# Performance work log

Measured on AMD Instinct MI355X. Metric: run time of the kernel, lower is better.

Reference implementation:

```python
import jax, jax.numpy as jnp
import numpy as np

B, N, INC, H, W = 1, 6, 256, 56, 100
DD, CC = 41, 64                         # depth bins (4..45 step 1), cam feat channels
NX, NY, NZ = 33, 33, 2                  # BEV grid from pc_range=[-50,-50,-5,50,50,3], grid=3
CZ = CC * NZ                            # 128 channels into bevencode
DXV = jnp.array([3.0, 3.0, 3.0], jnp.float32)
BXV = jnp.array([-48.5, -48.5, -3.5], jnp.float32)


def _frustum():
    ds = jnp.arange(4.0, 45.0, 1.0)                      # (41,)
    xs = jnp.linspace(0.0, 1599.0, W)
    ys = jnp.linspace(0.0, 899.0, H)
    d = jnp.broadcast_to(ds[:, None, None], (DD, H, W))
    xg = jnp.broadcast_to(xs[None, None, :], (DD, H, W))
    yg = jnp.broadcast_to(ys[None, :, None], (DD, H, W))
    return jnp.stack([xg, yg, d], -1)                    # (D,H,W,3)


def _conv(x, w):
    return jax.lax.conv_general_dilated(x, w, (1, 1), 'SAME',
                                        dimension_numbers=('NCHW', 'OIHW', 'NCHW'))


def _bn_relu(x, s, b, m, v):
    inv = s / jnp.sqrt(v + 1e-5)
    return jax.nn.relu(x * inv[None, :, None, None] + (b - m * inv)[None, :, None, None])


def _forward(x, rots, trans, dn_w, dn_b,
             bw1, bn1_s, bn1_b, bn1_m, bn1_v,
             bw2, bn2_s, bn2_b, bn2_m, bn2_v,
             bw3, bn3_s, bn3_b, bn3_m, bn3_v,
             bw4, bn4_s, bn4_b, bn4_m, bn4_v):
    # ---- CamEncode: 1x1 depthnet -> softmax depth dist + context features ----
    xf = x.reshape(B * N, INC, H, W)
    y = _conv(xf, dn_w) + dn_b[None, :, None, None]
    depth = jax.nn.softmax(y[:, :DD], axis=1).reshape(B, N, DD, H, W)
    feat = y[:, DD:DD + CC].reshape(B, N, CC, H, W)
    # ---- get_geometry: (u*d, v*d, d) -> ego frame ----
    fr = _frustum()                                                     # (D,H,W,3)
    pts = jnp.concatenate([fr[..., :2] * fr[..., 2:3], fr[..., 2:3]], -1)
    geom = jnp.einsum('bnij,dhwj->bndhwi', rots, pts) + trans[:, :, None, None, None, :]
    # ---- voxel indices (torch .long() truncates toward zero) ----
    coor = ((geom - (BXV - DXV / 2.0)) / DXV).astype(jnp.int32)         # (B,N,D,H,W,3)
    cx, cy, cz = coor[..., 0], coor[..., 1], coor[..., 2]
    kept = (cx >= 0) & (cx < NX) & (cy >= 0) & (cy < NY) & (cz >= 0) & (cz < NZ)
    bidx = jnp.arange(B, dtype=jnp.int32)[:, None, None, None, None]
    ranks = ((bidx * NZ + cz) * NY + cy) * NX + cx                      # bev rank per point
    nvox = B * NZ * NY * NX
    seg = jnp.where(kept, ranks, nvox).reshape(-1)                      # drop bucket = nvox
    # ---- lift: depth-weighted outer product, splat: segment-sum by voxel ----
    vol = depth[..., None] * feat.transpose(0, 1, 3, 4, 2)[:, :, None]  # (B,N,D,H,W,C)
    bev = jax.ops.segment_sum(vol.reshape(-1, CC), seg, num_segments=nvox + 1)[:nvox]
    bev = bev.reshape(B, NZ, NY, NX, CC).transpose(0, 4, 1, 2, 3).reshape(B, CZ, NY, NX)
    h = _bn_relu(_conv(bev, bw1), bn1_s, bn1_b, bn1_m, bn1_v)
    h = _bn_relu(_conv(h, bw2), bn2_s, bn2_b, bn2_m, bn2_v)
    h = _bn_relu(_conv(h, bw3), bn3_s, bn3_b, bn3_m, bn3_v)
    h = _bn_relu(_conv(h, bw4), bn4_s, bn4_b, bn4_m, bn4_v)
    return h                                                            # (B,256,33,33)


def setup_inputs() -> dict:
    key = jax.random.key(0)
    ks = jax.random.split(key, 16)
    x = jax.random.normal(ks[0], (B, N, INC, H, W), jnp.float32)
    # rots = small rotation perturbation composed with intrinsics inverse
    kinv = jnp.array([[1.0 / 800.0, 0.0, -1.0], [0.0, 1.0 / 800.0, -0.5625], [0.0, 0.0, 1.0]], jnp.float32)
    R = jnp.eye(3, dtype=jnp.float32) + 0.05 * jax.random.normal(ks[1], (B, N, 3, 3), jnp.float32)
    rots = jnp.einsum('bnij,jk->bnik', R, kinv)
    trans = 2.0 * jax.random.normal(ks[2], (B, N, 3), jnp.float32)

    def w(k, o, i, kh, kw):
        return jax.random.normal(k, (o, i, kh, kw), jnp.float32) * (2.0 / (i * kh * kw)) ** 0.5

    def bn(k, c):
        k1, k2, k3, k4 = jax.random.split(k, 4)
        return (1.0 + 0.1 * jax.random.normal(k1, (c,), jnp.float32),
                0.1 * jax.random.normal(k2, (c,), jnp.float32),
                0.1 * jax.random.normal(k3, (c,), jnp.float32),
                jax.random.uniform(k4, (c,), jnp.float32, 0.5, 1.5))
    bn1 = bn(ks[7], CZ); bn2 = bn(ks[8], 512); bn3 = bn(ks[9], 512); bn4 = bn(ks[10], 256)
    return dict(
        x=x, rots=rots, trans=trans,
        dn_w=w(ks[3], DD + CC, INC, 1, 1), dn_b=jnp.zeros((DD + CC,), jnp.float32),
        bw1=w(ks[4], CZ, CZ, 3, 3),
        bn1_s=bn1[0], bn1_b=bn1[1], bn1_m=bn1[2], bn1_v=bn1[3],
        bw2=w(ks[5], 512, CZ, 3, 3),
        bn2_s=bn2[0], bn2_b=bn2[1], bn2_m=bn2[2], bn2_v=bn2[3],
        bw3=w(ks[6], 512, 512, 3, 3),
        bn3_s=bn3[0], bn3_b=bn3[1], bn3_m=bn3[2], bn3_v=bn3[3],
        bw4=w(ks[11], 256, 512, 3, 3),
        bn4_s=bn4[0], bn4_b=bn4[1], bn4_m=bn4[2], bn4_v=bn4[3])


def reference(x, rots, trans, dn_w, dn_b,
              bw1, bn1_s, bn1_b, bn1_m, bn1_v,
              bw2, bn2_s, bn2_b, bn2_m, bn2_v,
              bw3, bn3_s, bn3_b, bn3_m, bn3_v,
              bw4, bn4_s, bn4_b, bn4_m, bn4_v):
    return _forward(x, rots, trans, dn_w, dn_b,
                    bw1, bn1_s, bn1_b, bn1_m, bn1_v,
                    bw2, bn2_s, bn2_b, bn2_m, bn2_v,
                    bw3, bn3_s, bn3_b, bn3_m, bn3_v,
                    bw4, bn4_s, bn4_b, bn4_m, bn4_v)
```

## Files before the change

### kernel.cpp

```cpp
#include <hip/hip_runtime.h>
#include <math.h>

#define NCAM  6
#define INC   256
#define HH    56
#define WW    100
#define HW    5600
#define NPIX  33600
#define DDEP  41
#define CFEAT 64
#define NCH   105
#define NXG   33
#define NYG   33
#define NZG   2
#define NVOX  2178
#define PADW  35
#define PADHW 1225
#define NPIXO 1089

typedef short bf16x8 __attribute__((ext_vector_type(8)));
typedef float f32x4  __attribute__((ext_vector_type(4)));

#define Y_OFF    0
#define Y_SZ     (NCAM * NCH * HW)
#define WDH_OFF  (Y_OFF + Y_SZ)
#define WDL_OFF  (WDH_OFF + 16384)
#define W1H_OFF  (WDL_OFF + 16384)
#define W1L_OFF  (W1H_OFF + 73728)
#define W2H_OFF  (W1L_OFF + 73728)
#define W2L_OFF  (W2H_OFF + 294912)
#define W3H_OFF  (W2L_OFF + 294912)
#define W3L_OFF  (W3H_OFF + 1179648)
#define W4H_OFF  (W3L_OFF + 1179648)
#define W4L_OFF  (W4H_OFF + 589824)
#define BEV_OFF  (W4L_OFF + 589824)
#define BEV_SZ   (NVOX * CFEAT)
#define A0H_OFF  (BEV_OFF + BEV_SZ)
#define A0L_OFF  (A0H_OFF + 78400)
#define A1H_OFF  (A0L_OFF + 78400)
#define A1L_OFF  (A1H_OFF + 78400)
#define A2H_OFF  (A1L_OFF + 78400)
#define A2L_OFF  (A2H_OFF + 313600)
#define A3H_OFF  (A2L_OFF + 313600)
#define A3L_OFF  (A3H_OFF + 313600)
#define P_OFF    (A3L_OFF + 313600)
#define P_SZ     4460544
#define WS_END   (P_OFF + P_SZ)

__device__ __forceinline__ unsigned short f2bf_rn(float f) {
    unsigned u = __builtin_bit_cast(unsigned, f);
    unsigned r = (u + 0x7FFFu + ((u >> 16) & 1u)) >> 16;
    return (unsigned short)r;
}
__device__ __forceinline__ void split_bf(float f, unsigned short& h, unsigned short& l) {
    h = f2bf_rn(f);
    float hf = __builtin_bit_cast(float, (unsigned)h << 16);
    l = f2bf_rn(f - hf);
}
__device__ __forceinline__ void split_bf_trunc(float f, short& h, short& l) {
    unsigned u = __builtin_bit_cast(unsigned, f);
    h = (short)(u >> 16);
    float hf = __builtin_bit_cast(float, u & 0xFFFF0000u);
    float r = f - hf;
    l = (short)(__builtin_bit_cast(unsigned, r) >> 16);
}

__device__ __forceinline__ void wprep_conv(const float* __restrict__ wgt,
                                           unsigned short* __restrict__ wh,
                                           unsigned short* __restrict__ wl,
                                           int COUT, int CIN, int i)
{
    int jj = i & 7, lane = (i >> 3) & 63;
    int r  = i >> 9;
    int nchk = CIN >> 5;
    int chk = r % nchk; r /= nchk;
    int ncog = COUT >> 4;
    int cog = r % ncog; int dydx = r / ncog;
    int co = cog * 16 + (lane & 15);
    int ci = chk * 32 + (lane >> 4) * 8 + jj;
    float w = wgt[((size_t)co * CIN + ci) * 9 + dydx];
    unsigned short h, l; split_bf(w, h, l);
    wh[i] = h; wl[i] = l;
}

__global__ __launch_bounds__(256) void k_wprep_all(const float* __restrict__ dnw,
                                                   const float* __restrict__ bw1,
                                                   const float* __restrict__ bw2,
                                                   const float* __restrict__ bw3,
                                                   const float* __restrict__ bw4,
                                                   unsigned short* __restrict__ wdh,
                                                   unsigned short* __restrict__ wdl,
                                                   unsigned short* __restrict__ w1h,
                                                   unsigned short* __restrict__ w1l,
                                                   unsigned short* __restrict__ w2h,
                                                   unsigned short* __restrict__ w2l,
                                                   unsigned short* __restrict__ w3h,
                                                   unsigned short* __restrict__ w3l,
                                                   unsigned short* __restrict__ w4h,
                                                   unsigned short* __restrict__ w4l)
{
    int i = blockIdx.x * 256 + threadIdx.x;
    if (i < 32768) {
        int jj = i & 7, lane = (i >> 3) & 63, chk = (i >> 9) & 7, ct = i >> 12;
        int co = ct * 16 + (lane & 15);
        int ci = chk * 32 + (lane >> 4) * 8 + jj;
        float w = (co < NCH) ? dnw[co * 256 + ci] : 0.f;
        unsigned short h, l; split_bf(w, h, l);
        wdh[i] = h; wdl[i] = l;
        return;
    }
    i -= 32768;
    if (i < 147456)  { wprep_conv(bw1, w1h, w1l, 128, 128, i); return; }
    i -= 147456;
    if (i < 589824)  { wprep_conv(bw2, w2h, w2l, 512, 128, i); return; }
    i -= 589824;
    if (i < 2359296) { wprep_conv(bw3, w3h, w3l, 512, 512, i); return; }
    i -= 2359296;
    if (i < 1179648) { wprep_conv(bw4, w4h, w4l, 256, 512, i); return; }
}

__global__ __launch_bounds__(256) void k_depthnet_fused(const float* __restrict__ x,
                                                        const unsigned short* __restrict__ wdh,
                                                        const unsigned short* __restrict__ wdl,
                                                        const float* __restrict__ dnb,
                                                        float* __restrict__ y)
{
    const int t  = threadIdx.x;
    const int w  = t >> 6;
    const int l  = t & 63;
    const int lp = l & 15;
    const int q  = l >> 4;
    const int n   = blockIdx.y;
    const int px  = blockIdx.x * 64 + w * 16 + lp;
    const bool pok = px < HW;
    const float* xl = x + (size_t)n * INC * HW + (pok ? px : 0);

    f32x4 acc[7];
#pragma unroll
    for (int ct = 0; ct < 7; ++ct) acc[ct] = (f32x4){0.f, 0.f, 0.f, 0.f};

#pragma unroll 2
    for (int ci0 = 0; ci0 < INC; ci0 += 32) {
        float bv[8];
#pragma unroll
        for (int jj = 0; jj < 8; ++jj)
            bv[jj] = xl[(size_t)(ci0 + q * 8 + jj) * HW];
        bf16x8 Bh, Bl;
#pragma unroll
        for (int jj = 0; jj < 8; ++jj) {
            short h, lo; split_bf_trunc(pok ? bv[jj] : 0.f, h, lo);
            Bh[jj] = h; Bl[jj] = lo;
        }
#pragma unroll
        for (int ct = 0; ct < 7; ++ct) {
            const size_t ab = (size_t)((ct * 8 + (ci0 >> 5)) * 64 + l) * 8;
            bf16x8 Ah = *(const bf16x8*)&wdh[ab];
            bf16x8 Al = *(const bf16x8*)&wdl[ab];
            acc[ct] = __builtin_amdgcn_mfma_f32_16x16x32_bf16(Ah, Bh, acc[ct], 0, 0, 0);
            acc[ct] = __builtin_amdgcn_mfma_f32_16x16x32_bf16(Ah, Bl, acc[ct], 0, 0, 0);
            acc[ct] = __builtin_amdgcn_mfma_f32_16x16x32_bf16(Al, Bh, acc[ct], 0, 0, 0);
        }
    }

    float v[4][4];
#pragma unroll
    for (int ct = 0; ct < 4; ++ct)
#pragma unroll
        for (int j = 0; j < 4; ++j) {
            int co = ct * 16 + q * 4 + j;
            v[ct][j] = acc[ct][j] + dnb[co];
        }

    {
        float m = -3.4e38f;
#pragma unroll
        for (int ct = 0; ct < 4; ++ct)
#pragma unroll
            for (int j = 0; j < 4; ++j) {
                int co = ct * 16 + q * 4 + j;
                if (co < DDEP) m = fmaxf(m, v[ct][j]);
            }
        m = fmaxf(m, __shfl_xor(m, 16));
        m = fmaxf(m, __shfl_xor(m, 32));
        float s = 0.f;
        float e[4][4];
#pragma unroll
        for (int ct = 0; ct < 4; ++ct)
#pragma unroll
            for (int j = 0; j < 4; ++j) {
                int co = ct * 16 + q * 4 + j;
                e[ct][j] = (co < DDEP) ? expf(v[ct][j] - m) : 0.f;
                s += e[ct][j];
            }
        s += __shfl_xor(s, 16);
        s += __shfl_xor(s, 32);
#pragma unroll
        for (int ct = 0; ct < 4; ++ct)
#pragma unroll
            for (int j = 0; j < 4; ++j) {
                int co = ct * 16 + q * 4 + j;
                if (co < DDEP) v[ct][j] = e[ct][j] / s;
            }
    }

    if (pok) {
#pragma unroll
        for (int ct = 0; ct < 4; ++ct)
#pragma unroll
            for (int j = 0; j < 4; ++j) {
                int co = ct * 16 + q * 4 + j;
                y[((size_t)n * NCH + co) * HW + px] = v[ct][j];
            }
#pragma unroll
        for (int ct = 4; ct < 7; ++ct)
#pragma unroll
            for (int j = 0; j < 4; ++j) {
                int co = ct * 16 + q * 4 + j;
                if (co < NCH)
                    y[((size_t)n * NCH + co) * HW + px] = acc[ct][j] + dnb[co];
            }
    }
}

__global__ __launch_bounds__(256) void k_splat2(const float* __restrict__ y,
                                                const float* __restrict__ rots,
                                                const float* __restrict__ trans,
                                                float* __restrict__ bev)
{
    __shared__ int vox[32 * DDEP];
    const int t  = threadIdx.x;
    const int p0 = blockIdx.x * 32;

    for (int k = t; k < 32 * DDEP; k += 256) {
        int pl = k / DDEP, d = k - pl * DDEP;
        int p = p0 + pl;
        int vx = -1;
        {
            int n = p / HW, hw = p - n * HW;
            int wi = hw % WW, hi = hw / WW;
            const float su = 1599.0f / 99.0f;
            const float sv = 899.0f / 55.0f;
            float u = __fmul_rn((float)wi, su);
            float v = __fmul_rn((float)hi, sv);
            const float* r = rots + n * 9;
            const float* tr = trans + n * 3;
            float dd  = 4.0f + (float)d;
            float pxv = __fmul_rn(u, dd);
            float pyv = __fmul_rn(v, dd);
            float gx = __fadd_rn(__fadd_rn(__fadd_rn(__fmul_rn(r[0], pxv), __fmul_rn(r[1], pyv)), __fmul_rn(r[2], dd)), tr[0]);
            float gy = __fadd_rn(__fadd_rn(__fadd_rn(__fmul_rn(r[3], pxv), __fmul_rn(r[4], pyv)), __fmul_rn(r[5], dd)), tr[1]);
            float gz = __fadd_rn(__fadd_rn(__fadd_rn(__fmul_rn(r[6], pxv), __fmul_rn(r[7], pyv)), __fmul_rn(r[8], dd)), tr[2]);
            int cx = (int)__fdiv_rn(__fadd_rn(gx, 50.0f), 3.0f);
            int cy = (int)__fdiv_rn(__fadd_rn(gy, 50.0f), 3.0f);
            int cz = (int)__fdiv_rn(__fadd_rn(gz, 5.0f), 3.0f);
            if (cx >= 0 && cx < NXG && cy >= 0 && cy < NYG && cz >= 0 && cz < NZG)
                vx = (cz * NYG + cy) * NXG + cx;
        }
        vox[k] = vx;
    }
    __syncthreads();

    const int g  = t >> 5;
    const int pl = t & 31;
    const int p  = p0 + pl;
    int n = p / HW, hw = p - n * HW;
    const float* dbase = y + (size_t)n * NCH * HW + hw;
    const float* fbase = dbase + (size_t)DDEP * HW;
    float f[8];
#pragma unroll
    for (int j = 0; j < 8; ++j) f[j] = fbase[(size_t)(g * 8 + j) * HW];

    float a[8];
#pragma unroll
    for (int j = 0; j < 8; ++j) a[j] = 0.f;
    int cur = -1;
    for (int d = 0; d < DDEP; ++d) {
        int vx = vox[pl * DDEP + d];
        if (vx != cur) {
            if (cur >= 0) {
                float* vp = bev + (size_t)cur * CFEAT + g * 8;
#pragma unroll
                for (int j = 0; j < 8; ++j) atomicAdd(vp + j, a[j]);
            }
            cur = vx;
#pragma unroll
            for (int j = 0; j < 8; ++j) a[j] = 0.f;
        }
        if (vx >= 0) {
            float dval = dbase[(size_t)d * HW];
#pragma unroll
            for (int j = 0; j < 8; ++j) a[j] += __fmul_rn(dval, f[j]);
        }
    }
    if (cur >= 0) {
        float* vp = bev + (size_t)cur * CFEAT + g * 8;
#pragma unroll
        for (int j = 0; j < 8; ++j) atomicAdd(vp + j, a[j]);
    }
}

__global__ __launch_bounds__(256) void k_bev2act(const float* __restrict__ bev,
                                                 unsigned short* __restrict__ ah,
                                                 unsigned short* __restrict__ al)
{
    int i = blockIdx.x * 256 + threadIdx.x;
    if (i >= NVOX * CFEAT) return;
    int vx = i >> 6, c = i & 63;
    int cz = vx / NPIXO, rem = vx - cz * NPIXO;
    int yy = rem / NXG, xx = rem - yy * NXG;
    int ch = c * 2 + cz;
    int pos = (yy + 1) * PADW + xx + 1;
    unsigned short h, l; split_bf(bev[i], h, l);
    ah[pos * 128 + ch] = h;
    al[pos * 128 + ch] = l;
}

template<int CIN, int COUT, int SL>
__global__ __launch_bounds__(256) void k_conv_mfma(const unsigned short* __restrict__ ah,
                                                   const unsigned short* __restrict__ al,
                                                   const unsigned short* __restrict__ wh,
                                                   const unsigned short* __restrict__ wl,
                                                   float* __restrict__ P)
{
    constexpr int CI_PER = CIN / SL;
    constexpr int CHUNKS = CI_PER / 32;
    constexpr int NSLOT  = CHUNKS * 8;
    constexpr int SMASK  = NSLOT - 1;
    constexpr int ROW    = CHUNKS * 64;
    constexpr int NCOB = COUT / 64;
    constexpr int G    = NCOB * SL;
    constexpr int GX   = G / 8;
    constexpr int POSN = 140;
    __shared__ unsigned short bs[POSN * ROW];
    const int t  = threadIdx.x;
    const int w  = t >> 6;
    const int l  = t & 63;
    const int lp = l & 15;
    const int q  = l >> 4;

    const int bid   = blockIdx.x;
    const int xcd   = bid & 7;
    const int slot  = bid >> 3;
    const int ytile = slot % 17;
    const int gon   = slot / 17;
    const int group = xcd * GX + gon;
    const int cobi  = group % NCOB;
    const int sl    = group / NCOB;

    const int y0  = ytile * 2;
    const int cob = cobi * 64 + w * 16;
    const int ci_base = sl * CI_PER;

    int  pos0[5];
    bool vld[5];
#pragma unroll
    for (int ct = 0; ct < 5; ++ct) {
        int tp = ct * 16 + lp;
        int r = tp / 33, c = tp - r * 33;
        bool v = (tp < 66) && (y0 + r < 33);
        vld[ct]  = v;
        pos0[ct] = v ? (r * 35 + c) : 0;
    }

    for (int i = t; i < POSN * NSLOT; i += 256) {
        int pos = i / NSLOT, s = i - pos * NSLOT;
        int gpos = y0 * 35 + pos;
        bool hi = s < CHUNKS * 4;
        int sq = hi ? s : s - CHUNKS * 4;
        int cio = (sq >> 2) * 32 + (sq & 3) * 8;
        const unsigned short* src = hi ? ah : al;
        int sp = s ^ (pos & SMASK);
        uint4 val = make_uint4(0u, 0u, 0u, 0u);
        if (gpos < PADHW)
            val = *(const uint4*)&src[(size_t)gpos * CIN + ci_base + cio];
        *(uint4*)&bs[pos * ROW + sp * 8] = val;
    }
    __syncthreads();

    f32x4 acc[5];
#pragma unroll
    for (int ct = 0; ct < 5; ++ct) acc[ct] = (f32x4){0.f, 0.f, 0.f, 0.f};

#pragma unroll 3
    for (int dydx = 0; dydx < 9; ++dydx) {
        int dy = dydx / 3, dx = dydx - dy * 3;
        int off = dy * 35 + dx;
        bf16x8 Ah[CHUNKS], Al[CHUNKS];
#pragma unroll
        for (int c = 0; c < CHUNKS; ++c) {
            const size_t abase = (size_t)(((dydx * (COUT >> 4) + (cob >> 4)) * (CIN >> 5)
                                           + (ci_base >> 5) + c) * 64 + l) * 8;
            Ah[c] = *(const bf16x8*)&wh[abase];
            Al[c] = *(const bf16x8*)&wl[abase];
        }
#pragma unroll
        for (int ct = 0; ct < 5; ++ct) {
            int pos = pos0[ct] + off;
#pragma unroll
            for (int c = 0; c < CHUNKS; ++c) {
                int sph = (c * 4 + q) ^ (pos & SMASK);
                bf16x8 Bh = *(const bf16x8*)&bs[pos * ROW + sph * 8];
                bf16x8 Bl = *(const bf16x8*)&bs[pos * ROW + (sph ^ (CHUNKS * 4)) * 8];
                acc[ct] = __builtin_amdgcn_mfma_f32_16x16x32_bf16(Ah[c], Bh, acc[ct], 0, 0, 0);
                acc[ct] = __builtin_amdgcn_mfma_f32_16x16x32_bf16(Ah[c], Bl, acc[ct], 0, 0, 0);
                acc[ct] = __builtin_amdgcn_mfma_f32_16x16x32_bf16(Al[c], Bh, acc[ct], 0, 0, 0);
            }
        }
    }

#pragma unroll
    for (int ct = 0; ct < 5; ++ct) {
        if (!vld[ct]) continue;
        int gp = y0 * 33 + ct * 16 + lp;
        float* dst = P + ((size_t)sl * NPIXO + gp) * COUT + cob + q * 4;
        *(f32x4*)dst = acc[ct];
    }
}

template<int SL>
__global__ __launch_bounds__(256) void k_finish(const float* __restrict__ P,
                                                const float* __restrict__ bns,
                                                const float* __restrict__ bnb,
                                                const float* __restrict__ bnm,
                                                const float* __restrict__ bnv,
                                                unsigned short* __restrict__ oh,
                                                unsigned short* __restrict__ ol,
                                                float* __restrict__ outf,
                                                int COUT)
{
    int i = blockIdx.x * 256 + threadIdx.x;
    if (i >= COUT * NPIXO) return;
    int co = i % COUT, p = i / COUT;
    float s = 0.f;
#pragma unroll
    for (int sl = 0; sl < SL; ++sl)
        s += P[((size_t)sl * NPIXO + p) * COUT + co];
    float sc = bns[co] / sqrtf(bnv[co] + 1e-5f);
    float bi = bnb[co] - bnm[co] * sc;
    float rv = fmaxf(fmaf(s, sc, bi), 0.f);
    if (outf) {
        outf[(size_t)co * NPIXO + p] = rv;
    } else {
        int yy = p / NXG, xx = p - yy * NXG;
        int pos = (yy + 1) * PADW + xx + 1;
        unsigned short h, lo; split_bf(rv, h, lo);
        oh[(size_t)pos * COUT + co] = h;
        ol[(size_t)pos * COUT + co] = lo;
    }
}

extern "C" void kernel_launch(void* const* d_in, const int* in_sizes, int n_in,
                              void* d_out, int out_size, void* d_ws, size_t ws_size,
                              hipStream_t stream)
{
    const float* x     = (const float*)d_in[0];
    const float* rots  = (const float*)d_in[1];
    const float* trans = (const float*)d_in[2];
    const float* dnw   = (const float*)d_in[3];
    const float* dnb   = (const float*)d_in[4];
    const float* bw1   = (const float*)d_in[5];
    const float* bn1s  = (const float*)d_in[6];
    const float* bn1b  = (const float*)d_in[7];
    const float* bn1m  = (const float*)d_in[8];
    const float* bn1v  = (const float*)d_in[9];
    const float* bw2   = (const float*)d_in[10];
    const float* bn2s  = (const float*)d_in[11];
    const float* bn2b  = (const float*)d_in[12];
    const float* bn2m  = (const float*)d_in[13];
    const float* bn2v  = (const float*)d_in[14];
    const float* bw3   = (const float*)d_in[15];
    const float* bn3s  = (const float*)d_in[16];
    const float* bn3b  = (const float*)d_in[17];
    const float* bn3m  = (const float*)d_in[18];
    const float* bn3v  = (const float*)d_in[19];
    const float* bw4   = (const float*)d_in[20];
    const float* bn4s  = (const float*)d_in[21];
    const float* bn4b  = (const float*)d_in[22];
    const float* bn4m  = (const float*)d_in[23];
    const float* bn4v  = (const float*)d_in[24];

    float* ws  = (float*)d_ws;
    float* y   = ws + Y_OFF;
    float* bev = ws + BEV_OFF;
    float* P   = ws + P_OFF;
    unsigned short* wdh = (unsigned short*)(ws + WDH_OFF);
    unsigned short* wdl = (unsigned short*)(ws + WDL_OFF);
    unsigned short* w1h = (unsigned short*)(ws + W1H_OFF);
    unsigned short* w1l = (unsigned short*)(ws + W1L_OFF);
    unsigned short* w2h = (unsigned short*)(ws + W2H_OFF);
    unsigned short* w2l = (unsigned short*)(ws + W2L_OFF);
    unsigned short* w3h = (unsigned short*)(ws + W3H_OFF);
    unsigned short* w3l = (unsigned short*)(ws + W3L_OFF);
    unsigned short* w4h = (unsigned short*)(ws + W4H_OFF);
    unsigned short* w4l = (unsigned short*)(ws + W4L_OFF);
    unsigned short* a0h = (unsigned short*)(ws + A0H_OFF);
    unsigned short* a0l = (unsigned short*)(ws + A0L_OFF);
    unsigned short* a1h = (unsigned short*)(ws + A1H_OFF);
    unsigned short* a1l = (unsigned short*)(ws + A1L_OFF);
    unsigned short* a2h = (unsigned short*)(ws + A2H_OFF);
    unsigned short* a2l = (unsigned short*)(ws + A2L_OFF);
    unsigned short* a3h = (unsigned short*)(ws + A3H_OFF);
    unsigned short* a3l = (unsigned short*)(ws + A3L_OFF);
    float* out = (float*)d_out;

    hipMemsetAsync(bev, 0, (size_t)(P_OFF - BEV_OFF) * sizeof(float), stream);

    k_wprep_all<<<16832, 256, 0, stream>>>(dnw, bw1, bw2, bw3, bw4,
                                           wdh, wdl, w1h, w1l, w2h, w2l,
                                           w3h, w3l, w4h, w4l);
    k_depthnet_fused<<<dim3(88, 6), 256, 0, stream>>>(x, wdh, wdl, dnb, y);
    k_splat2<<<1050, 256, 0, stream>>>(y, rots, trans, bev);

    k_bev2act<<<(NVOX * CFEAT + 255) / 256, 256, 0, stream>>>(bev, a0h, a0l);

    k_conv_mfma<128, 128, 4><<<136, 256, 0, stream>>>(a0h, a0l, w1h, w1l, P);
    k_finish<4><<<(128 * NPIXO + 255) / 256, 256, 0, stream>>>(P, bn1s, bn1b, bn1m, bn1v, a1h, a1l, nullptr, 128);
    k_conv_mfma<128, 512, 4><<<544, 256, 0, stream>>>(a1h, a1l, w2h, w2l, P);
    k_finish<4><<<(512 * NPIXO + 255) / 256, 256, 0, stream>>>(P, bn2s, bn2b, bn2m, bn2v, a2h, a2l, nullptr, 512);
    k_conv_mfma<512, 512, 8><<<1088, 256, 0, stream>>>(a2h, a2l, w3h, w3l, P);
    k_finish<8><<<(512 * NPIXO + 255) / 256, 256, 0, stream>>>(P, bn3s, bn3b, bn3m, bn3v, a3h, a3l, nullptr, 512);
    k_conv_mfma<512, 256, 8><<<544, 256, 0, stream>>>(a3h, a3l, w4h, w4l, P);
    k_finish<8><<<(256 * NPIXO + 255) / 256, 256, 0, stream>>>(P, bn4s, bn4b, bn4m, bn4v, nullptr, nullptr, out, 256);
}
```

Measured before the change: 137.6 us.

## Store conv activations as single bf16 and split depthnet channels across blocks

Activations feeding the BEV encoder convolutions are now stored as one rounded bf16 value instead of a hi/lo pair. This halves activation staging traffic and LDS footprint and drops one of three MFMAs per step, leaving weight hi/lo x activation. The depthnet kernel is also split over a z-dimension of 2 so each block computes 4 of the 7 channel tiles. The first z-slice handles the softmax channels. This adds parallelism and lowers register pressure, at the cost of reloading the input in both slices. Dropping the activation low part reduces accuracy, and the second depthnet slice computes one unused padding tile.

```diff
diff --git a/kernel.cpp b/kernel.cpp
--- a/kernel.cpp
+++ b/kernel.cpp
@@ -35,15 +35,11 @@
 #define W4L_OFF  (W4H_OFF + 589824)
 #define BEV_OFF  (W4L_OFF + 589824)
 #define BEV_SZ   (NVOX * CFEAT)
-#define A0H_OFF  (BEV_OFF + BEV_SZ)
-#define A0L_OFF  (A0H_OFF + 78400)
-#define A1H_OFF  (A0L_OFF + 78400)
-#define A1L_OFF  (A1H_OFF + 78400)
-#define A2H_OFF  (A1L_OFF + 78400)
-#define A2L_OFF  (A2H_OFF + 313600)
-#define A3H_OFF  (A2L_OFF + 313600)
-#define A3L_OFF  (A3H_OFF + 313600)
-#define P_OFF    (A3L_OFF + 313600)
+#define A0_OFF   (BEV_OFF + BEV_SZ)
+#define A1_OFF   (A0_OFF + 78400)
+#define A2_OFF   (A1_OFF + 78400)
+#define A3_OFF   (A2_OFF + 313600)
+#define P_OFF    (A3_OFF + 313600)
 #define P_SZ     4460544
 #define WS_END   (P_OFF + P_SZ)
 
@@ -131,13 +127,14 @@
     const int lp = l & 15;
     const int q  = l >> 4;
     const int n   = blockIdx.y;
+    const int ct0 = blockIdx.z * 4;
     const int px  = blockIdx.x * 64 + w * 16 + lp;
     const bool pok = px < HW;
     const float* xl = x + (size_t)n * INC * HW + (pok ? px : 0);
 
-    f32x4 acc[7];
-#pragma unroll
-    for (int ct = 0; ct < 7; ++ct) acc[ct] = (f32x4){0.f, 0.f, 0.f, 0.f};
+    f32x4 acc[4];
+#pragma unroll
+    for (int ct = 0; ct < 4; ++ct) acc[ct] = (f32x4){0.f, 0.f, 0.f, 0.f};
 
 #pragma unroll 2
     for (int ci0 = 0; ci0 < INC; ci0 += 32) {
@@ -152,8 +149,8 @@
             Bh[jj] = h; Bl[jj] = lo;
         }
 #pragma unroll
-        for (int ct = 0; ct < 7; ++ct) {
-            const size_t ab = (size_t)((ct * 8 + (ci0 >> 5)) * 64 + l) * 8;
+        for (int ct = 0; ct < 4; ++ct) {
+            const size_t ab = (size_t)(((ct0 + ct) * 8 + (ci0 >> 5)) * 64 + l) * 8;
             bf16x8 Ah = *(const bf16x8*)&wdh[ab];
             bf16x8 Al = *(const bf16x8*)&wdl[ab];
             acc[ct] = __builtin_amdgcn_mfma_f32_16x16x32_bf16(Ah, Bh, acc[ct], 0, 0, 0);
@@ -167,11 +164,11 @@
     for (int ct = 0; ct < 4; ++ct)
 #pragma unroll
         for (int j = 0; j < 4; ++j) {
-            int co = ct * 16 + q * 4 + j;
-            v[ct][j] = acc[ct][j] + dnb[co];
-        }
-
-    {
+            int co = (ct0 + ct) * 16 + q * 4 + j;
+            v[ct][j] = acc[ct][j] + ((co < NCH) ? dnb[co] : 0.f);
+        }
+
+    if (ct0 == 0) {
         float m = -3.4e38f;
 #pragma unroll
         for (int ct = 0; ct < 4; ++ct)
@@ -182,8 +179,8 @@
             }
         m = fmaxf(m, __shfl_xor(m, 16));
         m = fmaxf(m, __shfl_xor(m, 32));
+        float e[4][4];
         float s = 0.f;
-        float e[4][4];
 #pragma unroll
         for (int ct = 0; ct < 4; ++ct)
 #pragma unroll
@@ -208,16 +205,9 @@
         for (int ct = 0; ct < 4; ++ct)
 #pragma unroll
             for (int j = 0; j < 4; ++j) {
-                int co = ct * 16 + q * 4 + j;
-                y[((size_t)n * NCH + co) * HW + px] = v[ct][j];
-            }
-#pragma unroll
-        for (int ct = 4; ct < 7; ++ct)
-#pragma unroll
-            for (int j = 0; j < 4; ++j) {
-                int co = ct * 16 + q * 4 + j;
+                int co = (ct0 + ct) * 16 + q * 4 + j;
                 if (co < NCH)
-                    y[((size_t)n * NCH + co) * HW + px] = acc[ct][j] + dnb[co];
+                    y[((size_t)n * NCH + co) * HW + px] = v[ct][j];
             }
     }
 }
@@ -300,8 +290,7 @@
 }
 
 __global__ __launch_bounds__(256) void k_bev2act(const float* __restrict__ bev,
-                                                 unsigned short* __restrict__ ah,
-                                                 unsigned short* __restrict__ al)
+                                                 unsigned short* __restrict__ a0)
 {
     int i = blockIdx.x * 256 + threadIdx.x;
     if (i >= NVOX * CFEAT) return;
@@ -310,23 +299,20 @@
     int yy = rem / NXG, xx = rem - yy * NXG;
     int ch = c * 2 + cz;
     int pos = (yy + 1) * PADW + xx + 1;
-    unsigned short h, l; split_bf(bev[i], h, l);
-    ah[pos * 128 + ch] = h;
-    al[pos * 128 + ch] = l;
+    a0[pos * 128 + ch] = f2bf_rn(bev[i]);
 }
 
 template<int CIN, int COUT, int SL>
-__global__ __launch_bounds__(256) void k_conv_mfma(const unsigned short* __restrict__ ah,
-                                                   const unsigned short* __restrict__ al,
+__global__ __launch_bounds__(256) void k_conv_mfma(const unsigned short* __restrict__ act,
                                                    const unsigned short* __restrict__ wh,
                                                    const unsigned short* __restrict__ wl,
                                                    float* __restrict__ P)
 {
     constexpr int CI_PER = CIN / SL;
     constexpr int CHUNKS = CI_PER / 32;
-    constexpr int NSLOT  = CHUNKS * 8;
+    constexpr int NSLOT  = CHUNKS * 4;
     constexpr int SMASK  = NSLOT - 1;
-    constexpr int ROW    = CHUNKS * 64;
+    constexpr int ROW    = NSLOT * 8;
     constexpr int NCOB = COUT / 64;
     constexpr int G    = NCOB * SL;
     constexpr int GX   = G / 8;
@@ -365,14 +351,10 @@
     for (int i = t; i < POSN * NSLOT; i += 256) {
         int pos = i / NSLOT, s = i - pos * NSLOT;
         int gpos = y0 * 35 + pos;
-        bool hi = s < CHUNKS * 4;
-        int sq = hi ? s : s - CHUNKS * 4;
-        int cio = (sq >> 2) * 32 + (sq & 3) * 8;
-        const unsigned short* src = hi ? ah : al;
         int sp = s ^ (pos & SMASK);
         uint4 val = make_uint4(0u, 0u, 0u, 0u);
         if (gpos < PADHW)
-            val = *(const uint4*)&src[(size_t)gpos * CIN + ci_base + cio];
+            val = *(const uint4*)&act[(size_t)gpos * CIN + ci_base + s * 8];
         *(uint4*)&bs[pos * ROW + sp * 8] = val;
     }
     __syncthreads();
@@ -399,11 +381,9 @@
 #pragma unroll
             for (int c = 0; c < CHUNKS; ++c) {
                 int sph = (c * 4 + q) ^ (pos & SMASK);
-                bf16x8 Bh = *(const bf16x8*)&bs[pos * ROW + sph * 8];
-                bf16x8 Bl = *(const bf16x8*)&bs[pos * ROW + (sph ^ (CHUNKS * 4)) * 8];
-                acc[ct] = __builtin_amdgcn_mfma_f32_16x16x32_bf16(Ah[c], Bh, acc[ct], 0, 0, 0);
-                acc[ct] = __builtin_amdgcn_mfma_f32_16x16x32_bf16(Ah[c], Bl, acc[ct], 0, 0, 0);
-                acc[ct] = __builtin_amdgcn_mfma_f32_16x16x32_bf16(Al[c], Bh, acc[ct], 0, 0, 0);
+                bf16x8 B = *(const bf16x8*)&bs[pos * ROW + sph * 8];
+                acc[ct] = __builtin_amdgcn_mfma_f32_16x16x32_bf16(Ah[c], B, acc[ct], 0, 0, 0);
+                acc[ct] = __builtin_amdgcn_mfma_f32_16x16x32_bf16(Al[c], B, acc[ct], 0, 0, 0);
             }
         }
     }
@@ -423,8 +403,7 @@
                                                 const float* __restrict__ bnb,
                                                 const float* __restrict__ bnm,
                                                 const float* __restrict__ bnv,
-                                                unsigned short* __restrict__ oh,
-                                                unsigned short* __restrict__ ol,
+                                                unsigned short* __restrict__ oact,
                                                 float* __restrict__ outf,
                                                 int COUT)
 {
@@ -443,9 +422,7 @@
     } else {
         int yy = p / NXG, xx = p - yy * NXG;
         int pos = (yy + 1) * PADW + xx + 1;
-        unsigned short h, lo; split_bf(rv, h, lo);
-        oh[(size_t)pos * COUT + co] = h;
-        ol[(size_t)pos * COUT + co] = lo;
+        oact[(size_t)pos * COUT + co] = f2bf_rn(rv);
     }
 }
 
@@ -493,14 +470,10 @@
     unsigned short* w3l = (unsigned short*)(ws + W3L_OFF);
     unsigned short* w4h = (unsigned short*)(ws + W4H_OFF);
     unsigned short* w4l = (unsigned short*)(ws + W4L_OFF);
-    unsigned short* a0h = (unsigned short*)(ws + A0H_OFF);
-    unsigned short* a0l = (unsigned short*)(ws + A0L_OFF);
-    unsigned short* a1h = (unsigned short*)(ws + A1H_OFF);
-    unsigned short* a1l = (unsigned short*)(ws + A1L_OFF);
-    unsigned short* a2h = (unsigned short*)(ws + A2H_OFF);
-    unsigned short* a2l = (unsigned short*)(ws + A2L_OFF);
-    unsigned short* a3h = (unsigned short*)(ws + A3H_OFF);
-    unsigned short* a3l = (unsigned short*)(ws + A3L_OFF);
+    unsigned short* a0  = (unsigned short*)(ws + A0_OFF);
+    unsigned short* a1  = (unsigned short*)(ws + A1_OFF);
+    unsigned short* a2  = (unsigned short*)(ws + A2_OFF);
+    unsigned short* a3  = (unsigned short*)(ws + A3_OFF);
     float* out = (float*)d_out;
 
     hipMemsetAsync(bev, 0, (size_t)(P_OFF - BEV_OFF) * sizeof(float), stream);
@@ -508,17 +481,17 @@
     k_wprep_all<<<16832, 256, 0, stream>>>(dnw, bw1, bw2, bw3, bw4,
                                            wdh, wdl, w1h, w1l, w2h, w2l,
                                            w3h, w3l, w4h, w4l);
-    k_depthnet_fused<<<dim3(88, 6), 256, 0, stream>>>(x, wdh, wdl, dnb, y);
+    k_depthnet_fused<<<dim3(88, 6, 2), 256, 0, stream>>>(x, wdh, wdl, dnb, y);
     k_splat2<<<1050, 256, 0, stream>>>(y, rots, trans, bev);
 
-    k_bev2act<<<(NVOX * CFEAT + 255) / 256, 256, 0, stream>>>(bev, a0h, a0l);
-
-    k_conv_mfma<128, 128, 4><<<136, 256, 0, stream>>>(a0h, a0l, w1h, w1l, P);
-    k_finish<4><<<(128 * NPIXO + 255) / 256, 256, 0, stream>>>(P, bn1s, bn1b, bn1m, bn1v, a1h, a1l, nullptr, 128);
-    k_conv_mfma<128, 512, 4><<<544, 256, 0, stream>>>(a1h, a1l, w2h, w2l, P);
-    k_finish<4><<<(512 * NPIXO + 255) / 256, 256, 0, stream>>>(P, bn2s, bn2b, bn2m, bn2v, a2h, a2l, nullptr, 512);
-    k_conv_mfma<512, 512, 8><<<1088, 256, 0, stream>>>(a2h, a2l, w3h, w3l, P);
-    k_finish<8><<<(512 * NPIXO + 255) / 256, 256, 0, stream>>>(P, bn3s, bn3b, bn3m, bn3v, a3h, a3l, nullptr, 512);
-    k_conv_mfma<512, 256, 8><<<544, 256, 0, stream>>>(a3h, a3l, w4h, w4l, P);
-    k_finish<8><<<(256 * NPIXO + 255) / 256, 256, 0, stream>>>(P, bn4s, bn4b, bn4m, bn4v, nullptr, nullptr, out, 256);
-}
+    k_bev2act<<<(NVOX * CFEAT + 255) / 256, 256, 0, stream>>>(bev, a0);
+
+    k_conv_mfma<128, 128, 4><<<136, 256, 0, stream>>>(a0, w1h, w1l, P);
+    k_finish<4><<<(128 * NPIXO + 255) / 256, 256, 0, stream>>>(P, bn1s, bn1b, bn1m, bn1v, a1, nullptr, 128);
+    k_conv_mfma<128, 512, 4><<<544, 256, 0, stream>>>(a1, w2h, w2l, P);
+    k_finish<4><<<(512 * NPIXO + 255) / 256, 256, 0, stream>>>(P, bn2s, bn2b, bn2m, bn2v, a2, nullptr, 512);
+    k_conv_mfma<512, 512, 8><<<1088, 256, 0, stream>>>(a2, w3h, w3l, P);
+    k_finish<8><<<(512 * NPIXO + 255) / 256, 256, 0, stream>>>(P, bn3s, bn3b, bn3m, bn3v, a3, nullptr, 512);
+    k_conv_mfma<512, 256, 8><<<544, 256, 0, stream>>>(a3, w4h, w4l, P);
+    k_finish<8><<<(256 * NPIXO + 255) / 256, 256, 0, stream>>>(P, bn4s, bn4b, bn4m, bn4v, nullptr, out, 256);
+}
```

New measurement: 118.3 us. -14.0%, faster.
